# Performance work log

Hardware: AMD Instinct MI355X
Metric: run time of the kernel (lower is better)

## Reference

```python
import jax, jax.numpy as jnp
import numpy as np
from jax import lax

B, T, D, H = 32, 512, 1024, 1024


def setup_inputs() -> dict:
    key = jax.random.key(0)
    ks = jax.random.split(key, 11)
    s = 0.02  # truncated_normal-ish scale
    inp = {
        'x': jax.random.normal(ks[0], (B, T, D), jnp.float32),
        'W_i': jax.random.normal(ks[1], (D, H), jnp.float32) * s,
        'U_i': jax.random.normal(ks[2], (H, H), jnp.float32) * s,
        'W_f': jax.random.normal(ks[3], (D, H), jnp.float32) * s,
        'U_f': jax.random.normal(ks[4], (H, H), jnp.float32) * s,
        'W_g': jax.random.normal(ks[5], (D, H), jnp.float32) * s,
        'U_g': jax.random.normal(ks[6], (H, H), jnp.float32) * s,
        'W_c': jax.random.normal(ks[7], (D, H), jnp.float32) * s,
        'U_c': jax.random.normal(ks[8], (H, H), jnp.float32) * s,
        'W_o': jax.random.normal(ks[9], (H, H), jnp.float32) * s,
        'b_i': jnp.zeros((H,), jnp.float32),
        'b_f': jnp.zeros((H,), jnp.float32),
        'b_g': jnp.zeros((H,), jnp.float32),
        'b_c': jnp.zeros((H,), jnp.float32),
        'b_o': jnp.zeros((H,), jnp.float32),
    }
    return inp


def reference(x, W_i, U_i, W_f, U_f, W_g, U_g, W_c, U_c, W_o,
              b_i, b_f, b_g, b_c, b_o):
    Bx, Tx, Dx = x.shape
    Hx = W_i.shape[1]
    # Fuse the 4 input-to-gate GEMMs (done once over the whole sequence)
    W = jnp.concatenate([W_i, W_f, W_g, W_c], axis=1)   # [D, 4H]
    U = jnp.concatenate([U_i, U_f, U_g, U_c], axis=1)   # [H, 4H]
    b = jnp.concatenate([b_i, b_f, b_g, b_c])           # [4H]
    xt = jnp.transpose(x, (1, 0, 2))                    # [T, B, D] time-major
    x_proj = jnp.einsum('tbd,dg->tbg', xt, W) + b       # [T, B, 4H]

    def step(carry, xp):
        h, c = carry
        z = xp + h @ U                                  # fused recurrent GEMM
        zi, zf, zg, zc = jnp.split(z, 4, axis=-1)
        i = jax.nn.sigmoid(zi)
        f = jax.nn.sigmoid(zf)
        g = jax.nn.sigmoid(zg)          # NB: module applies nonlin_i (sigmoid) to g
        c_tilda = jnp.tanh(zc)
        c = f * c + i * c_tilda
        h = g * jnp.tanh(c)
        return (h, c), h

    h0 = jnp.zeros((Bx, Hx), x.dtype)
    _, states = lax.scan(step, (h0, h0), x_proj)        # states: [T, B, H]
    out = jax.nn.relu(jnp.einsum('tbh,ho->tbo', states, W_o) + b_o)
    return jnp.transpose(out, (1, 0, 2))                # [B, T, H]
```

## Files before the change

kernel.cpp:

```cpp
#include <hip/hip_runtime.h>

#define OFF_H      0ull
#define OFF_C      65536ull
#define OFF_BAR    98304ull
#define OFF_XPC    131072ull
#define OFF_STATES 4325376ull

#define BAR_REL    8192
#define BAR_DUMP   16384

#define AL(p) __hip_atomic_load((p), __ATOMIC_RELAXED, __HIP_MEMORY_SCOPE_AGENT)
#define AS(p, v) __hip_atomic_store((p), (v), __ATOMIC_RELAXED, __HIP_MEMORY_SCOPE_AGENT)

#define GLOAD4(dst, ptr) \
    asm volatile("global_load_dwordx4 %0, %1, off sc0 sc1" \
                 : "=v"(dst) : "v"(ptr) : "memory")
#define GLOADF(dst, ptr) \
    asm volatile("global_load_dword %0, %1, off sc0 sc1" \
                 : "=v"(dst) : "v"(ptr) : "memory")
#define GLOADI(dst, ptr) \
    asm volatile("global_load_dword %0, %1, off sc0 sc1" \
                 : "=v"(dst) : "v"(ptr) : "memory")

#define WAIT_VMN_(n) asm volatile("s_waitcnt vmcnt(" #n ")" ::: "memory")
#define WAIT_VMN(n) do { WAIT_VMN_(n); __builtin_amdgcn_sched_barrier(0); } while (0)

#define BARRIER_LDS() do { asm volatile("s_waitcnt lgkmcnt(0)" ::: "memory"); \
    __builtin_amdgcn_s_barrier(); \
    __builtin_amdgcn_sched_barrier(0); } while (0)

static __device__ inline float sigmoidf_(float x) { return 1.f / (1.f + __expf(-x)); }
static __device__ inline float tanhf_(float x) { return 1.f - 2.f / (1.f + __expf(2.f * x)); }

__global__ __launch_bounds__(256) void k_init(float* hb, float* cs, int* bar) {
    int i = blockIdx.x * 256 + threadIdx.x;
    hb[i] = 0.f;
    if (i < 32768) cs[i] = 0.f;
    if (i < 16384) bar[i] = 0;
}

__global__ __launch_bounds__(256) void k_gemm0(
    const float* __restrict__ x,
    const float* __restrict__ Wi, const float* __restrict__ Wf,
    const float* __restrict__ Wg, const float* __restrict__ Wc,
    const float* __restrict__ bi, const float* __restrict__ bfv,
    const float* __restrict__ bg, const float* __restrict__ bc,
    float* __restrict__ xpc, int t0)
{
    __shared__ float Ash[16 * 128];
    __shared__ float Bsh[16 * 128];
    int tid = threadIdx.x;
    int bm = blockIdx.x >> 5, bn = blockIdx.x & 31;
    int r0 = bm * 128, n0 = bn * 128;
    int gate = bn >> 3;
    int nloc = (bn & 7) * 128;
    const float* W; const float* bias;
    if (gate == 0)      { W = Wi; bias = bi; }
    else if (gate == 1) { W = Wf; bias = bfv; }
    else if (gate == 2) { W = Wg; bias = bg; }
    else                { W = Wc; bias = bc; }

    int mg = tid >> 4, ng = tid & 15;
    int m0 = mg * 8, n0l = ng * 8;
    int sm = tid >> 1, skh = (tid & 1) * 8;
    int sk = tid >> 4, snof = (tid & 15) * 8;
    int Ra = r0 + sm;
    const float* aptr = x + (size_t)(Ra & 31) * 524288
                          + (size_t)(t0 + (Ra >> 5)) * 1024 + skh;

    float acc[8][8];
    for (int i = 0; i < 8; i++)
        for (int j = 0; j < 8; j++) acc[i][j] = 0.f;

    for (int k0 = 0; k0 < 1024; k0 += 16) {
        float4 av0 = *(const float4*)(aptr + k0);
        float4 av1 = *(const float4*)(aptr + k0 + 4);
        float4 bv0 = *(const float4*)(W + (size_t)(k0 + sk) * 1024 + nloc + snof);
        float4 bv1 = *(const float4*)(W + (size_t)(k0 + sk) * 1024 + nloc + snof + 4);
        Ash[(skh + 0) * 128 + sm] = av0.x;
        Ash[(skh + 1) * 128 + sm] = av0.y;
        Ash[(skh + 2) * 128 + sm] = av0.z;
        Ash[(skh + 3) * 128 + sm] = av0.w;
        Ash[(skh + 4) * 128 + sm] = av1.x;
        Ash[(skh + 5) * 128 + sm] = av1.y;
        Ash[(skh + 6) * 128 + sm] = av1.z;
        Ash[(skh + 7) * 128 + sm] = av1.w;
        *(float4*)&Bsh[sk * 128 + snof] = bv0;
        *(float4*)&Bsh[sk * 128 + snof + 4] = bv1;
        __syncthreads();
#pragma unroll
        for (int k = 0; k < 16; k++) {
            float4 a0 = *(const float4*)&Ash[k * 128 + m0];
            float4 a1 = *(const float4*)&Ash[k * 128 + m0 + 4];
            float4 b0 = *(const float4*)&Bsh[k * 128 + n0l];
            float4 b1 = *(const float4*)&Bsh[k * 128 + n0l + 4];
            float aa[8], bb[8];
            aa[0] = a0.x; aa[1] = a0.y; aa[2] = a0.z; aa[3] = a0.w;
            aa[4] = a1.x; aa[5] = a1.y; aa[6] = a1.z; aa[7] = a1.w;
            bb[0] = b0.x; bb[1] = b0.y; bb[2] = b0.z; bb[3] = b0.w;
            bb[4] = b1.x; bb[5] = b1.y; bb[6] = b1.z; bb[7] = b1.w;
#pragma unroll
            for (int i = 0; i < 8; i++)
#pragma unroll
                for (int j = 0; j < 8; j++)
                    acc[i][j] = __builtin_fmaf(aa[i], bb[j], acc[i][j]);
        }
        __syncthreads();
    }
    float fbs[8];
#pragma unroll
    for (int j = 0; j < 8; j++) fbs[j] = bias[nloc + n0l + j];
    for (int i = 0; i < 8; i++) {
        size_t rowoff = (size_t)(r0 + m0 + i) * 4096 + n0 + n0l;
#pragma unroll
        for (int j = 0; j < 8; j++)
            xpc[rowoff + j] = acc[i][j] + fbs[j];
    }
}

__global__ __launch_bounds__(128, 2) void k_scan32(
    const float* __restrict__ Ui, const float* __restrict__ Uf,
    const float* __restrict__ Ug, const float* __restrict__ Uc,
    const float* __restrict__ xpc,
    float* hbuf, float* cstate, float* states, int* bar, int t0)
{
    int tid = threadIdx.x;

    if (blockIdx.x == 512) {
        if (tid < 64) {
            int endv = (t0 + 32) * 8;
            for (;;) {
                int m = 0x7fffffff;
#pragma unroll
                for (int i = 0; i < 8; i++)
                    m = min(m, AL(&bar[(tid + i * 64) * 16]));
                m = min(m, __shfl_xor(m, 1, 64));
                m = min(m, __shfl_xor(m, 2, 64));
                m = min(m, __shfl_xor(m, 4, 64));
                m = min(m, __shfl_xor(m, 8, 64));
                m = min(m, __shfl_xor(m, 16, 64));
                m = min(m, __shfl_xor(m, 32, 64));
                if (tid < 16) AS(&bar[BAR_REL + tid * 64], m);
                if (m >= endv) break;
            }
        }
        return;
    }

    __shared__ float hsh[2][4][1024];
    __shared__ float zfin[2][32];
    __shared__ float csh[64];

    int wv = tid >> 6;
    int ku = tid & 63;
    int col0 = ((((blockIdx.x & 7) << 6) | (blockIdx.x >> 3)) << 1);
    const float* Bu0 = (wv == 0) ? Ui : Ug;
    const float* Bu1 = (wv == 0) ? Uf : Uc;

    float4 ur[2][2][4];
#pragma unroll
    for (int gl = 0; gl < 2; gl++) {
        const float* Bu = gl ? Bu1 : Bu0;
#pragma unroll
        for (int c = 0; c < 2; c++)
#pragma unroll
            for (int j = 0; j < 4; j++) {
                size_t kb = (size_t)(j * 256 + ku * 4);
                float4 u;
                u.x = Bu[(kb + 0) * 1024 + col0 + c];
                u.y = Bu[(kb + 1) * 1024 + col0 + c];
                u.z = Bu[(kb + 2) * 1024 + col0 + c];
                u.w = Bu[(kb + 3) * 1024 + col0 + c];
                ur[gl][c][j] = u;
            }
    }

    if (tid < 8) {
        for (int p = 0; p < 8; p++)
            csh[p * 8 + tid] = cstate[(size_t)(p * 4 + (tid >> 1)) * 1024 + col0 + (tid & 1)];
    }

    int* gml = &bar[BAR_REL + (blockIdx.x & 15) * 64];
    float* dumpA = (float*)&bar[BAR_DUMP + ((blockIdx.x & 63) << 6) + (tid & 63)];
    float* dumpB = (float*)&bar[BAR_DUMP + 4096 + ((blockIdx.x & 63) << 6) + (tid & 63)];

    int rA = AL(gml);
    int rB = rA;
    float4 gA[8], gB[8];
    float xgA[4], xgB[4];

#define STAGE(g, xg, rv, Qv)                                                  \
    if ((Qv) < 256) {                                                         \
        int need_ = t0 * 8 + (Qv) - 7;                                        \
        if (rv < need_) {             \
            int s_;                                                           \
            for (;;) { s_ = AL(gml); if (s_ >= need_) break;                  \
                       __builtin_amdgcn_s_sleep(1); }                         \
            rv = s_;                                                          \
        }                                                                     \
        const float* hb_ = hbuf + (size_t)((((Qv) >> 3)) & 1) * 32768         \
                         + (size_t)(((Qv) & 7) * 4) * 1024;                   \
        _Pragma("unroll")                                                     \
        for (int q = 0; q < 8; q++) {                                         \
            int idx = tid + q * 128;                                          \
            const float* p_ = hb_ + (size_t)(idx >> 8) * 1024 + (idx & 255) * 4; \
            GLOAD4(g[q], p_);                                                 \
        }                                                                     \
        if (tid < 64) {           \
            int o_ = tid & 7;                                                 \
            const float* xr = xpc + (size_t)((((Qv) >> 3) * 32) + ((Qv) & 7) * 4 \
                            + (o_ >> 1)) * 4096 + col0 + (o_ & 1);            \
            GLOADF(xg[0], xr);                                                \
            GLOADF(xg[1], xr + 1024);                                         \
            GLOADF(xg[2], xr + 2048);                                         \
            GLOADF(xg[3], xr + 3072);                                         \
        }                                                                     \
        GLOADI(rv, gml);                \
    }

#define COMMIT(g, Qv, FIRST)                                                  \
    {                                                                         \
        if (tid < 64) { if (FIRST) { WAIT_VMN(13); } else { WAIT_VMN(15); } } \
        else          { WAIT_VMN(9); }                                        \
        if (!(FIRST) && (Qv) >= 2 && tid == 0)                                \
            AS(&bar[blockIdx.x * 16], t0 * 8 + (Qv) - 1);                     \
        _Pragma("unroll")                                                     \
        for (int q = 0; q < 8; q++) {                                         \
            int idx = tid + q * 128;                                          \
            *(float4*)&hsh[(Qv) & 1][idx >> 8][(idx & 255) * 4] = g[q];       \
        }                                                                     \
        BARRIER_LDS();                                                        \
    }

#define PASS(Qv, xg)                                                          \
    {                                                                         \
        int tt_ = (Qv) >> 3, p_ = (Qv) & 7;                                   \
        float w_[16];                                                         \
        _Pragma("unroll")                                                     \
        for (int v = 0; v < 16; v++) w_[v] = 0.f;                             \
        _Pragma("unroll")                                                     \
        for (int b = 0; b < 4; b++) {                                         \
            _Pragma("unroll")                                                 \
            for (int j = 0; j < 4; j++) {                                     \
                float4 hv = *(const float4*)&hsh[(Qv) & 1][b][j * 256 + ku * 4]; \
                _Pragma("unroll")                                             \
                for (int gl = 0; gl < 2; gl++)                                \
                _Pragma("unroll")                                             \
                for (int c = 0; c < 2; c++) {                                 \
                    float4 u = ur[gl][c][j];                                  \
                    int v = b * 4 + gl * 2 + c;                               \
                    w_[v] = __builtin_fmaf(hv.x, u.x, w_[v]);                 \
                    w_[v] = __builtin_fmaf(hv.y, u.y, w_[v]);                 \
                    w_[v] = __builtin_fmaf(hv.z, u.z, w_[v]);                 \
                    w_[v] = __builtin_fmaf(hv.w, u.w, w_[v]);                 \
                }                                                             \
            }                                                                 \
        }                                                                     \
         \
        float u_[8];                                                          \
        _Pragma("unroll")                                                     \
        for (int i = 0; i < 8; i++) {                                         \
            float a = w_[2 * i], b = w_[2 * i + 1];                           \
            float x = (ku & 1) ? a : b;                                       \
            float y = __shfl_xor(x, 1, 64);                                   \
            u_[i] = ((ku & 1) ? b : a) + y;                                   \
        }                                                                     \
        float v_[4];                                                          \
        _Pragma("unroll")                                                     \
        for (int i = 0; i < 4; i++) {                                         \
            float a = u_[2 * i], b = u_[2 * i + 1];                           \
            float x = (ku & 2) ? a : b;                                       \
            float y = __shfl_xor(x, 2, 64);                                   \
            v_[i] = ((ku & 2) ? b : a) + y;                                   \
        }                                                                     \
        float s_[2];                                                          \
        _Pragma("unroll")                                                     \
        for (int i = 0; i < 2; i++) {                                         \
            float a = v_[2 * i], b = v_[2 * i + 1];                           \
            float x = (ku & 4) ? a : b;                                       \
            float y = __shfl_xor(x, 4, 64);                                   \
            s_[i] = ((ku & 4) ? b : a) + y;                                   \
        }                                                                     \
        float r_;                                                             \
        {                                                                     \
            float a = s_[0], b = s_[1];                                       \
            float x = (ku & 8) ? a : b;                                       \
            float y = __shfl_xor(x, 8, 64);                                   \
            r_ = ((ku & 8) ? b : a) + y;                                      \
        }                                                                     \
        r_ += __shfl_xor(r_, 16, 64);                                         \
        r_ += __shfl_xor(r_, 32, 64);                                         \
        if (ku < 16)                                                          \
            zfin[(Qv) & 1][(ku >> 2) * 8 + (ku & 1) * 4 + wv * 2 + ((ku >> 1) & 1)] = r_; \
        BARRIER_LDS();                                                        \
        if (tid < 64) {              \
            int o_ = tid & 7;                                                 \
            int b8 = (o_ >> 1) * 8, c4 = (o_ & 1) * 4;                        \
            float zi = zfin[(Qv) & 1][b8 + c4 + 0] + xg[0];                   \
            float zf = zfin[(Qv) & 1][b8 + c4 + 1] + xg[1];                   \
            float zg = zfin[(Qv) & 1][b8 + c4 + 2] + xg[2];                   \
            float zc = zfin[(Qv) & 1][b8 + c4 + 3] + xg[3];                   \
            float ig = sigmoidf_(zi);                                         \
            float fg = sigmoidf_(zf);                                         \
            float gg = sigmoidf_(zg);            \
            float ct = tanhf_(zc);                                            \
            float cv = fg * csh[p_ * 8 + o_] + ig * ct;                       \
            if (tid < 8) csh[p_ * 8 + tid] = cv;                              \
            float hv2 = gg * tanhf_(cv);                                      \
            int t_ = t0 + tt_;                                                \
            int bg_ = p_ * 4 + (o_ >> 1);                                     \
            float* ha_ = (tid < 8)                                            \
                ? &hbuf[(size_t)((t_ + 1) & 1) * 32768 + (size_t)bg_ * 1024 + col0 + (o_ & 1)] \
                : dumpA;                                                      \
            AS(ha_, hv2);                                                     \
            float* sa_ = (tid < 8)                                            \
                ? &states[((size_t)t_ * 32 + bg_) * 1024 + col0 + (o_ & 1)]   \
                : dumpB;                                                      \
            *sa_ = hv2;                                                       \
        }                                                                     \
    }

    STAGE(gA, xgA, rA, 0)
    STAGE(gB, xgB, rB, 1)
    COMMIT(gA, 0, 1)

#pragma unroll 1
    for (int Q = 0; Q < 256; Q += 2) {
        PASS(Q, xgA)
        STAGE(gA, xgA, rA, Q + 2)
        COMMIT(gB, Q + 1, 0)
        PASS(Q + 1, xgB)
        STAGE(gB, xgB, rB, Q + 3)
        if (Q + 2 < 256) { COMMIT(gA, Q + 2, 0) }
    }

    WAIT_VMN(0);
    if (tid == 0) AS(&bar[blockIdx.x * 16], t0 * 8 + 256);

    if (tid < 8) {
        for (int p = 0; p < 8; p++)
            cstate[(size_t)(p * 4 + (tid >> 1)) * 1024 + col0 + (tid & 1)] = csh[p * 8 + tid];
    }
#undef STAGE
#undef COMMIT
#undef PASS
}

__global__ __launch_bounds__(256) void k_gemm1(
    const float* __restrict__ A, const float* __restrict__ Wo,
    const float* __restrict__ bo, float* __restrict__ outp)
{
    __shared__ float Ash[16 * 128];
    __shared__ float Bsh[16 * 128];
    int tid = threadIdx.x;
    int bm = blockIdx.x >> 3, bn = blockIdx.x & 7;
    int r0 = bm * 128, n0 = bn * 128;
    int mg = tid >> 4, ng = tid & 15;
    int m0 = mg * 8, n0l = ng * 8;
    int sm = tid >> 1, skh = (tid & 1) * 8;
    int sk = tid >> 4, snof = (tid & 15) * 8;
    const float* aptr = A + (size_t)(r0 + sm) * 1024 + skh;

    float acc[8][8];
    for (int i = 0; i < 8; i++)
        for (int j = 0; j < 8; j++) acc[i][j] = 0.f;

    for (int k0 = 0; k0 < 1024; k0 += 16) {
        float4 av0 = *(const float4*)(aptr + k0);
        float4 av1 = *(const float4*)(aptr + k0 + 4);
        float4 bv0 = *(const float4*)(Wo + (size_t)(k0 + sk) * 1024 + n0 + snof);
        float4 bv1 = *(const float4*)(Wo + (size_t)(k0 + sk) * 1024 + n0 + snof + 4);
        Ash[(skh + 0) * 128 + sm] = av0.x;
        Ash[(skh + 1) * 128 + sm] = av0.y;
        Ash[(skh + 2) * 128 + sm] = av0.z;
        Ash[(skh + 3) * 128 + sm] = av0.w;
        Ash[(skh + 4) * 128 + sm] = av1.x;
        Ash[(skh + 5) * 128 + sm] = av1.y;
        Ash[(skh + 6) * 128 + sm] = av1.z;
        Ash[(skh + 7) * 128 + sm] = av1.w;
        *(float4*)&Bsh[sk * 128 + snof] = bv0;
        *(float4*)&Bsh[sk * 128 + snof + 4] = bv1;
        __syncthreads();
#pragma unroll
        for (int k = 0; k < 16; k++) {
            float4 a0 = *(const float4*)&Ash[k * 128 + m0];
            float4 a1 = *(const float4*)&Ash[k * 128 + m0 + 4];
            float4 b0 = *(const float4*)&Bsh[k * 128 + n0l];
            float4 b1 = *(const float4*)&Bsh[k * 128 + n0l + 4];
            float aa[8], bb[8];
            aa[0] = a0.x; aa[1] = a0.y; aa[2] = a0.z; aa[3] = a0.w;
            aa[4] = a1.x; aa[5] = a1.y; aa[6] = a1.z; aa[7] = a1.w;
            bb[0] = b0.x; bb[1] = b0.y; bb[2] = b0.z; bb[3] = b0.w;
            bb[4] = b1.x; bb[5] = b1.y; bb[6] = b1.z; bb[7] = b1.w;
#pragma unroll
            for (int i = 0; i < 8; i++)
#pragma unroll
                for (int j = 0; j < 8; j++)
                    acc[i][j] = __builtin_fmaf(aa[i], bb[j], acc[i][j]);
        }
        __syncthreads();
    }
    float fbs[8];
#pragma unroll
    for (int j = 0; j < 8; j++) fbs[j] = bo[n0 + n0l + j];
    for (int i = 0; i < 8; i++) {
        int R = r0 + m0 + i;
        size_t rowoff = (size_t)(R & 31) * 524288 + (size_t)(R >> 5) * 1024 + n0 + n0l;
#pragma unroll
        for (int j = 0; j < 8; j++) {
            float v = acc[i][j] + fbs[j];
            outp[rowoff + j] = v > 0.f ? v : 0.f;
        }
    }
}

extern "C" void kernel_launch(void* const* d_in, const int* in_sizes, int n_in,
                              void* d_out, int out_size, void* d_ws, size_t ws_size,
                              hipStream_t stream)
{
    const float* x   = (const float*)d_in[0];
    const float* Wi  = (const float*)d_in[1];
    const float* Ui  = (const float*)d_in[2];
    const float* Wf  = (const float*)d_in[3];
    const float* Uf  = (const float*)d_in[4];
    const float* Wg  = (const float*)d_in[5];
    const float* Ug  = (const float*)d_in[6];
    const float* Wc  = (const float*)d_in[7];
    const float* Uc  = (const float*)d_in[8];
    const float* Wo  = (const float*)d_in[9];
    const float* bi  = (const float*)d_in[10];
    const float* bfv = (const float*)d_in[11];
    const float* bg  = (const float*)d_in[12];
    const float* bc  = (const float*)d_in[13];
    const float* bo  = (const float*)d_in[14];

    float* ws     = (float*)d_ws;
    float* hbuf   = ws + OFF_H;
    float* cstate = ws + OFF_C;
    int*   bar    = (int*)(ws + OFF_BAR);
    float* xpc    = ws + OFF_XPC;
    float* states = ws + OFF_STATES;
    float* outp   = (float*)d_out;

    k_init<<<256, 256, 0, stream>>>(hbuf, cstate, bar);
    for (int c = 0; c < 16; c++) {
        k_gemm0<<<256, 256, 0, stream>>>(x, Wi, Wf, Wg, Wc, bi, bfv, bg, bc,
                                         xpc, c * 32);
        k_scan32<<<513, 128, 0, stream>>>(Ui, Uf, Ug, Uc, xpc,
                                          hbuf, cstate, states, bar, c * 32);
    }
    k_gemm1<<<1024, 256, 0, stream>>>(states, Wo, bo, outp);
}
```

Measured before the change: 10.60 ms.

## Halve scan block count with 256-thread blocks covering four columns and 8-row passes

After: 8.702 ms. 17.9% less time.

```diff
diff --git a/kernel.cpp b/kernel.cpp
--- a/kernel.cpp
+++ b/kernel.cpp
@@ -7,7 +7,6 @@
 #define OFF_STATES 4325376ull
 
 #define BAR_REL    8192
-#define BAR_DUMP   16384
 
 #define AL(p) __hip_atomic_load((p), __ATOMIC_RELAXED, __HIP_MEMORY_SCOPE_AGENT)
 #define AS(p, v) __hip_atomic_store((p), (v), __ATOMIC_RELAXED, __HIP_MEMORY_SCOPE_AGENT)
@@ -118,7 +117,7 @@
     }
 }
 
-__global__ __launch_bounds__(128, 2) void k_scan32(
+__global__ __launch_bounds__(256, 1) void k_scan32(
     const float* __restrict__ Ui, const float* __restrict__ Uf,
     const float* __restrict__ Ug, const float* __restrict__ Uc,
     const float* __restrict__ xpc,
@@ -126,14 +125,15 @@
 {
     int tid = threadIdx.x;
 
-    if (blockIdx.x == 512) {
+    if (blockIdx.x == 256) {
         if (tid < 64) {
-            int endv = (t0 + 32) * 8;
+            int endv = t0 * 4 + 128;
             for (;;) {
-                int m = 0x7fffffff;
-#pragma unroll
-                for (int i = 0; i < 8; i++)
-                    m = min(m, AL(&bar[(tid + i * 64) * 16]));
+                int m0 = AL(&bar[(tid * 4 + 0) * 16]);
+                int m1 = AL(&bar[(tid * 4 + 1) * 16]);
+                int m2 = AL(&bar[(tid * 4 + 2) * 16]);
+                int m3 = AL(&bar[(tid * 4 + 3) * 16]);
+                int m = min(min(m0, m1), min(m2, m3));
                 m = min(m, __shfl_xor(m, 1, 64));
                 m = min(m, __shfl_xor(m, 2, 64));
                 m = min(m, __shfl_xor(m, 4, 64));
@@ -147,86 +147,85 @@
         return;
     }
 
-    __shared__ float hsh[2][4][1024];
-    __shared__ float zfin[2][32];
-    __shared__ float csh[64];
+    __shared__ float hsh[2][8][1024];
+    __shared__ float zfin[2][128];
+    __shared__ float csh[4][32];
 
     int wv = tid >> 6;
     int ku = tid & 63;
-    int col0 = ((((blockIdx.x & 7) << 6) | (blockIdx.x >> 3)) << 1);
-    const float* Bu0 = (wv == 0) ? Ui : Ug;
-    const float* Bu1 = (wv == 0) ? Uf : Uc;
+    int gp = wv & 1, cp = wv >> 1;
+    int col0 = ((((blockIdx.x & 7) << 5) | (blockIdx.x >> 3)) << 2);
 
     float4 ur[2][2][4];
-#pragma unroll
-    for (int gl = 0; gl < 2; gl++) {
-        const float* Bu = gl ? Bu1 : Bu0;
-#pragma unroll
-        for (int c = 0; c < 2; c++)
-#pragma unroll
-            for (int j = 0; j < 4; j++) {
-                size_t kb = (size_t)(j * 256 + ku * 4);
-                float4 u;
-                u.x = Bu[(kb + 0) * 1024 + col0 + c];
-                u.y = Bu[(kb + 1) * 1024 + col0 + c];
-                u.z = Bu[(kb + 2) * 1024 + col0 + c];
-                u.w = Bu[(kb + 3) * 1024 + col0 + c];
-                ur[gl][c][j] = u;
+    {
+        const float* Bu0 = (gp == 0) ? Ui : Ug;
+        const float* Bu1 = (gp == 0) ? Uf : Uc;
+#pragma unroll
+        for (int gl = 0; gl < 2; gl++) {
+            const float* Bu = gl ? Bu1 : Bu0;
+#pragma unroll
+            for (int cl = 0; cl < 2; cl++) {
+                int c = col0 + cp * 2 + cl;
+#pragma unroll
+                for (int j = 0; j < 4; j++) {
+                    size_t kb = (size_t)(j * 256 + ku * 4);
+                    float4 u;
+                    u.x = Bu[(kb + 0) * 1024 + c];
+                    u.y = Bu[(kb + 1) * 1024 + c];
+                    u.z = Bu[(kb + 2) * 1024 + c];
+                    u.w = Bu[(kb + 3) * 1024 + c];
+                    ur[gl][cl][j] = u;
+                }
             }
-    }
-
-    if (tid < 8) {
-        for (int p = 0; p < 8; p++)
-            csh[p * 8 + tid] = cstate[(size_t)(p * 4 + (tid >> 1)) * 1024 + col0 + (tid & 1)];
+        }
+    }
+
+    if (tid < 32) {
+        for (int p = 0; p < 4; p++)
+            csh[p][tid] = cstate[(size_t)(p * 8 + (tid >> 2)) * 1024 + col0 + (tid & 3)];
     }
 
     int* gml = &bar[BAR_REL + (blockIdx.x & 15) * 64];
-    float* dumpA = (float*)&bar[BAR_DUMP + ((blockIdx.x & 63) << 6) + (tid & 63)];
-    float* dumpB = (float*)&bar[BAR_DUMP + 4096 + ((blockIdx.x & 63) << 6) + (tid & 63)];
-
-    int rA = AL(gml);
-    int rB = rA;
+    int rv = AL(gml);
     float4 gA[8], gB[8];
     float xgA[4], xgB[4];
 
-#define STAGE(g, xg, rv, Qv)                                                  \
-    if ((Qv) < 256) {                                                         \
-        int need_ = t0 * 8 + (Qv) - 7;                                        \
+#define STAGE(g, xg, Qv)                                                      \
+    if ((Qv) < 128) {                                                         \
+        int need_ = t0 * 4 + (Qv) - 3;                                        \
         if (rv < need_) {             \
             int s_;                                                           \
             for (;;) { s_ = AL(gml); if (s_ >= need_) break;                  \
                        __builtin_amdgcn_s_sleep(1); }                         \
             rv = s_;                                                          \
         }                                                                     \
-        const float* hb_ = hbuf + (size_t)((((Qv) >> 3)) & 1) * 32768         \
-                         + (size_t)(((Qv) & 7) * 4) * 1024;                   \
+        const float* hb_ = hbuf + (size_t)(((Qv) >> 2) & 1) * 32768           \
+                         + (size_t)(((Qv) & 3) * 8) * 1024;                   \
         _Pragma("unroll")                                                     \
         for (int q = 0; q < 8; q++) {                                         \
-            int idx = tid + q * 128;                                          \
+            int idx = tid + q * 256;                                          \
             const float* p_ = hb_ + (size_t)(idx >> 8) * 1024 + (idx & 255) * 4; \
             GLOAD4(g[q], p_);                                                 \
         }                                                                     \
-        if (tid < 64) {           \
-            int o_ = tid & 7;                                                 \
-            const float* xr = xpc + (size_t)((((Qv) >> 3) * 32) + ((Qv) & 7) * 4 \
-                            + (o_ >> 1)) * 4096 + col0 + (o_ & 1);            \
+        if (tid < 32) {    \
+            const float* xr = xpc + (size_t)((((Qv) >> 2) * 32) + ((Qv) & 3) * 8 \
+                            + (tid >> 2)) * 4096 + col0 + (tid & 3);          \
             GLOADF(xg[0], xr);                                                \
             GLOADF(xg[1], xr + 1024);                                         \
             GLOADF(xg[2], xr + 2048);                                         \
             GLOADF(xg[3], xr + 3072);                                         \
         }                                                                     \
-        GLOADI(rv, gml);                \
-    }
-
-#define COMMIT(g, Qv, FIRST)                                                  \
+        GLOADI(rv, gml);        \
+    }
+
+#define COMMIT(g, Qv, N0, N1)                                                 \
     {                                                                         \
-        if (tid < 64) { if (FIRST) { WAIT_VMN(13); } else { WAIT_VMN(15); } } \
-        else          { WAIT_VMN(9); }                                        \
-        if (!(FIRST) && (Qv) >= 2 && tid == 0)                                \
-            AS(&bar[blockIdx.x * 16], t0 * 8 + (Qv) - 1);                     \
+        if (tid < 64) { WAIT_VMN(N0); } else { WAIT_VMN(N1); }                \
+        if ((Qv) >= 2 && tid == 0)                                            \
+            AS(&bar[blockIdx.x * 16], t0 * 4 + (Qv) - 1);                     \
         _Pragma("unroll")                                                     \
         for (int q = 0; q < 8; q++) {                                         \
-            int idx = tid + q * 128;                                          \
+            int idx = tid + q * 256;                                          \
             *(float4*)&hsh[(Qv) & 1][idx >> 8][(idx & 255) * 4] = g[q];       \
         }                                                                     \
         BARRIER_LDS();                                                        \
@@ -234,21 +233,21 @@
 
 #define PASS(Qv, xg)                                                          \
     {                                                                         \
-        int tt_ = (Qv) >> 3, p_ = (Qv) & 7;                                   \
-        float w_[16];                                                         \
-        _Pragma("unroll")                                                     \
-        for (int v = 0; v < 16; v++) w_[v] = 0.f;                             \
-        _Pragma("unroll")                                                     \
-        for (int b = 0; b < 4; b++) {                                         \
+        int tt_ = (Qv) >> 2, p_ = (Qv) & 3;                                   \
+        float w_[32];                                                         \
+        _Pragma("unroll")                                                     \
+        for (int v = 0; v < 32; v++) w_[v] = 0.f;                             \
+        _Pragma("unroll")                                                     \
+        for (int b = 0; b < 8; b++) {                                         \
             _Pragma("unroll")                                                 \
             for (int j = 0; j < 4; j++) {                                     \
                 float4 hv = *(const float4*)&hsh[(Qv) & 1][b][j * 256 + ku * 4]; \
                 _Pragma("unroll")                                             \
                 for (int gl = 0; gl < 2; gl++)                                \
                 _Pragma("unroll")                                             \
-                for (int c = 0; c < 2; c++) {                                 \
-                    float4 u = ur[gl][c][j];                                  \
-                    int v = b * 4 + gl * 2 + c;                               \
+                for (int cl = 0; cl < 2; cl++) {                              \
+                    float4 u = ur[gl][cl][j];                                 \
+                    int v = b * 4 + gl * 2 + cl;                              \
                     w_[v] = __builtin_fmaf(hv.x, u.x, w_[v]);                 \
                     w_[v] = __builtin_fmaf(hv.y, u.y, w_[v]);                 \
                     w_[v] = __builtin_fmaf(hv.z, u.z, w_[v]);                 \
@@ -256,90 +255,99 @@
                 }                                                             \
             }                                                                 \
         }                                                                     \
-         \
-        float u_[8];                                                          \
-        _Pragma("unroll")                                                     \
-        for (int i = 0; i < 8; i++) {                                         \
+                    \
+        float u_[16];                                                         \
+        _Pragma("unroll")                                                     \
+        for (int i = 0; i < 16; i++) {                                        \
             float a = w_[2 * i], b = w_[2 * i + 1];                           \
             float x = (ku & 1) ? a : b;                                       \
             float y = __shfl_xor(x, 1, 64);                                   \
             u_[i] = ((ku & 1) ? b : a) + y;                                   \
         }                                                                     \
-        float v_[4];                                                          \
-        _Pragma("unroll")                                                     \
-        for (int i = 0; i < 4; i++) {                                         \
+        float v_[8];                                                          \
+        _Pragma("unroll")                                                     \
+        for (int i = 0; i < 8; i++) {                                         \
             float a = u_[2 * i], b = u_[2 * i + 1];                           \
             float x = (ku & 2) ? a : b;                                       \
             float y = __shfl_xor(x, 2, 64);                                   \
             v_[i] = ((ku & 2) ? b : a) + y;                                   \
         }                                                                     \
-        float s_[2];                                                          \
-        _Pragma("unroll")                                                     \
-        for (int i = 0; i < 2; i++) {                                         \
+        float s_[4];                                                          \
+        _Pragma("unroll")                                                     \
+        for (int i = 0; i < 4; i++) {                                         \
             float a = v_[2 * i], b = v_[2 * i + 1];                           \
             float x = (ku & 4) ? a : b;                                       \
             float y = __shfl_xor(x, 4, 64);                                   \
             s_[i] = ((ku & 4) ? b : a) + y;                                   \
         }                                                                     \
-        float r_;                                                             \
-        {                                                                     \
-            float a = s_[0], b = s_[1];                                       \
+        float r_[2];                                                          \
+        _Pragma("unroll")                                                     \
+        for (int i = 0; i < 2; i++) {                                         \
+            float a = s_[2 * i], b = s_[2 * i + 1];                           \
             float x = (ku & 8) ? a : b;                                       \
             float y = __shfl_xor(x, 8, 64);                                   \
-            r_ = ((ku & 8) ? b : a) + y;                                      \
-        }                                                                     \
-        r_ += __shfl_xor(r_, 16, 64);                                         \
-        r_ += __shfl_xor(r_, 32, 64);                                         \
-        if (ku < 16)                                                          \
-            zfin[(Qv) & 1][(ku >> 2) * 8 + (ku & 1) * 4 + wv * 2 + ((ku >> 1) & 1)] = r_; \
+            r_[i] = ((ku & 8) ? b : a) + y;                                   \
+        }                                                                     \
+        float q_;                                                             \
+        {                                                                     \
+            float a = r_[0], b = r_[1];                                       \
+            float x = (ku & 16) ? a : b;                                      \
+            float y = __shfl_xor(x, 16, 64);                                  \
+            q_ = ((ku & 16) ? b : a) + y;                                     \
+        }                                                                     \
+        q_ += __shfl_xor(q_, 32, 64);                                         \
+                 \
+        if (ku < 32)                                                          \
+            zfin[(Qv) & 1][((ku >> 2) & 7) * 16 + (gp * 2 + ((ku >> 1) & 1)) * 4 \
+                           + cp * 2 + (ku & 1)] = q_;                         \
         BARRIER_LDS();                                                        \
-        if (tid < 64) {              \
-            int o_ = tid & 7;                                                 \
-            int b8 = (o_ >> 1) * 8, c4 = (o_ & 1) * 4;                        \
-            float zi = zfin[(Qv) & 1][b8 + c4 + 0] + xg[0];                   \
-            float zf = zfin[(Qv) & 1][b8 + c4 + 1] + xg[1];                   \
-            float zg = zfin[(Qv) & 1][b8 + c4 + 2] + xg[2];                   \
-            float zc = zfin[(Qv) & 1][b8 + c4 + 3] + xg[3];                   \
+        if (tid < 32) {                    \
+            int b8 = (tid >> 2) * 16, c4 = tid & 3;                           \
+            float zi = zfin[(Qv) & 1][b8 + 0 + c4] + xg[0];                   \
+            float zf = zfin[(Qv) & 1][b8 + 4 + c4] + xg[1];                   \
+            float zg = zfin[(Qv) & 1][b8 + 8 + c4] + xg[2];                   \
+            float zc = zfin[(Qv) & 1][b8 + 12 + c4] + xg[3];                  \
             float ig = sigmoidf_(zi);                                         \
             float fg = sigmoidf_(zf);                                         \
             float gg = sigmoidf_(zg);            \
             float ct = tanhf_(zc);                                            \
-            float cv = fg * csh[p_ * 8 + o_] + ig * ct;                       \
-            if (tid < 8) csh[p_ * 8 + tid] = cv;                              \
+            float cv = fg * csh[p_][tid] + ig * ct;                           \
+            csh[p_][tid] = cv;                                                \
             float hv2 = gg * tanhf_(cv);                                      \
             int t_ = t0 + tt_;                                                \
-            int bg_ = p_ * 4 + (o_ >> 1);                                     \
-            float* ha_ = (tid < 8)                                            \
-                ? &hbuf[(size_t)((t_ + 1) & 1) * 32768 + (size_t)bg_ * 1024 + col0 + (o_ & 1)] \
-                : dumpA;                                                      \
-            AS(ha_, hv2);                                                     \
-            float* sa_ = (tid < 8)                                            \
-                ? &states[((size_t)t_ * 32 + bg_) * 1024 + col0 + (o_ & 1)]   \
-                : dumpB;                                                      \
-            *sa_ = hv2;                                                       \
-        }                                                                     \
-    }
-
-    STAGE(gA, xgA, rA, 0)
-    STAGE(gB, xgB, rB, 1)
-    COMMIT(gA, 0, 1)
+            int bg_ = p_ * 8 + (tid >> 2);                                    \
+            AS(&hbuf[(size_t)((t_ + 1) & 1) * 32768 + (size_t)bg_ * 1024      \
+                     + col0 + c4], hv2);                                      \
+            states[((size_t)t_ * 32 + bg_) * 1024 + col0 + c4] = hv2;         \
+        }                                                                     \
+    }
+
+    STAGE(gA, xgA, 0)
+    STAGE(gB, xgB, 1)
+    COMMIT(gA, 0, 13, 9) PASS(0, xgA) STAGE(gA, xgA, 2)
+    COMMIT(gB, 1, 15, 9) PASS(1, xgB) STAGE(gB, xgB, 3)
+    COMMIT(gA, 2, 15, 9) PASS(2, xgA) STAGE(gA, xgA, 4)
+    COMMIT(gB, 3, 16, 9) PASS(3, xgB) STAGE(gB, xgB, 5)
 
 #pragma unroll 1
-    for (int Q = 0; Q < 256; Q += 2) {
+    for (int Q = 4; Q < 126; Q += 2) {
+        COMMIT(gA, Q, 16, 9)
         PASS(Q, xgA)
-        STAGE(gA, xgA, rA, Q + 2)
-        COMMIT(gB, Q + 1, 0)
+        STAGE(gA, xgA, Q + 2)
+        COMMIT(gB, Q + 1, 16, 9)
         PASS(Q + 1, xgB)
-        STAGE(gB, xgB, rB, Q + 3)
-        if (Q + 2 < 256) { COMMIT(gA, Q + 2, 0) }
-    }
+        STAGE(gB, xgB, Q + 3)
+    }
+
+    COMMIT(gA, 126, 16, 9) PASS(126, xgA)
+    COMMIT(gB, 127, 0, 0)  PASS(127, xgB)
 
     WAIT_VMN(0);
-    if (tid == 0) AS(&bar[blockIdx.x * 16], t0 * 8 + 256);
-
-    if (tid < 8) {
-        for (int p = 0; p < 8; p++)
-            cstate[(size_t)(p * 4 + (tid >> 1)) * 1024 + col0 + (tid & 1)] = csh[p * 8 + tid];
+    if (tid == 0) AS(&bar[blockIdx.x * 16], t0 * 4 + 128);
+
+    if (tid < 32) {
+        for (int p = 0; p < 4; p++)
+            cstate[(size_t)(p * 8 + (tid >> 2)) * 1024 + col0 + (tid & 3)] = csh[p][tid];
     }
 #undef STAGE
 #undef COMMIT
@@ -446,7 +454,7 @@
     for (int c = 0; c < 16; c++) {
         k_gemm0<<<256, 256, 0, stream>>>(x, Wi, Wf, Wg, Wc, bi, bfv, bg, bc,
                                          xpc, c * 32);
-        k_scan32<<<513, 128, 0, stream>>>(Ui, Uf, Ug, Uc, xpc,
+        k_scan32<<<257, 256, 0, stream>>>(Ui, Uf, Ug, Uc, xpc,
                                           hbuf, cstate, states, bar, c * 32);
     }
     k_gemm1<<<1024, 256, 0, stream>>>(states, Wo, bo, outp);
```
